# Performance work log

Hardware: AMD Instinct MI355X
Metric: run time of the kernel (lower is better)

Reference implementation:

```python
import jax, jax.numpy as jnp
import numpy as np

N_EMBD = 1024
N_HEAD = 16
HEAD_SIZE = N_EMBD // N_HEAD
EPS = 1e-5


def _layernorm(x, g, b):
    m = x.mean(-1, keepdims=True)
    v = x.var(-1, keepdims=True)
    return (x - m) / jnp.sqrt(v + EPS) * g + b


def _mha(q_in, kv_in, wq, wk, wv, pw, pb, causal):
    # q_in: [B,T,C], kv_in: [B,S,C]; per-head Linear projections fused into one matmul.
    B, T, C = q_in.shape
    S = kv_in.shape[1]
    H, hd = N_HEAD, HEAD_SIZE
    q = (q_in @ wq).reshape(B, T, H, hd)
    k = (kv_in @ wk).reshape(B, S, H, hd)
    v = (kv_in @ wv).reshape(B, S, H, hd)
    scale = 1.0 / np.sqrt(hd).astype(np.float32)
    wei = jnp.einsum('bthd,bshd->bhts', q, k) * scale  # [B,H,T,S]
    if causal:
        mask = jnp.tril(jnp.ones((T, S), dtype=bool))
        wei = jnp.where(mask, wei, -jnp.inf)
    attn = jax.nn.softmax(wei, axis=-1)
    out = jnp.einsum('bhts,bshd->bthd', attn, v).reshape(B, T, C)
    return out @ pw + pb


def setup_inputs() -> dict:
    key = jax.random.key(0)
    ks = jax.random.split(key, 20)
    C = N_EMBD
    B, T, S = 8, 1024, 1024
    s = 0.02
    inp = {
        'x': jax.random.normal(ks[0], (B, T, C), jnp.float32),
        'encoder_output': jax.random.normal(ks[1], (B, S, C), jnp.float32),
        # self-attention (per-head q/k/v Linears concatenated head-major -> [C, C])
        'sa_wq': jax.random.normal(ks[2], (C, C), jnp.float32) * s,
        'sa_wk': jax.random.normal(ks[3], (C, C), jnp.float32) * s,
        'sa_wv': jax.random.normal(ks[4], (C, C), jnp.float32) * s,
        'sa_pw': jax.random.normal(ks[5], (C, C), jnp.float32) * s,
        'sa_pb': jnp.zeros((C,), jnp.float32),
        # cross-attention
        'ca_wq': jax.random.normal(ks[6], (C, C), jnp.float32) * s,
        'ca_wk': jax.random.normal(ks[7], (C, C), jnp.float32) * s,
        'ca_wv': jax.random.normal(ks[8], (C, C), jnp.float32) * s,
        'ca_pw': jax.random.normal(ks[9], (C, C), jnp.float32) * s,
        'ca_pb': jnp.zeros((C,), jnp.float32),
        # feed-forward
        'ff_w1': jax.random.normal(ks[10], (C, 4 * C), jnp.float32) * s,
        'ff_b1': jnp.zeros((4 * C,), jnp.float32),
        'ff_w2': jax.random.normal(ks[11], (4 * C, C), jnp.float32) * s,
        'ff_b2': jnp.zeros((C,), jnp.float32),
        # layernorms
        'ln1_g': jnp.ones((C,), jnp.float32), 'ln1_b': jnp.zeros((C,), jnp.float32),
        'ln2_g': jnp.ones((C,), jnp.float32), 'ln2_b': jnp.zeros((C,), jnp.float32),
        'ln3_g': jnp.ones((C,), jnp.float32), 'ln3_b': jnp.zeros((C,), jnp.float32),
    }
    return inp


def reference(x, encoder_output, sa_wq, sa_wk, sa_wv, sa_pw, sa_pb,
              ca_wq, ca_wk, ca_wv, ca_pw, ca_pb,
              ff_w1, ff_b1, ff_w2, ff_b2,
              ln1_g, ln1_b, ln2_g, ln2_b, ln3_g, ln3_b):
    # self-attn: q from ln1(x), but k/v from raw residual x (memory=x in source)
    x = x + _mha(_layernorm(x, ln1_g, ln1_b), x, sa_wq, sa_wk, sa_wv, sa_pw, sa_pb, causal=True)
    # cross-attn: q from ln2(x), k/v from encoder_output, no mask
    x = x + _mha(_layernorm(x, ln2_g, ln2_b), encoder_output, ca_wq, ca_wk, ca_wv, ca_pw, ca_pb, causal=False)
    # feed-forward: Linear -> ReLU -> Linear
    h = _layernorm(x, ln3_g, ln3_b)
    x = x + (jax.nn.relu(h @ ff_w1 + ff_b1) @ ff_w2 + ff_b2)
    return x
```

## Files before the change

### kernel.cpp

```cpp
#include <hip/hip_runtime.h>
#include <stdint.h>
#include <stddef.h>

typedef __bf16 bf16_t;
typedef __bf16 bf16x4 __attribute__((ext_vector_type(4)));
typedef __bf16 bf16x8 __attribute__((ext_vector_type(8)));
typedef float f32x4 __attribute__((ext_vector_type(4)));

#define DEV static __device__ __forceinline__

static constexpr int kB = 8, kT = 1024, kC = 1024, kM = 8192, kH = 16, kHD = 64, kFF = 4096;

DEV f32x4 mfma16(bf16x8 a, bf16x8 b, f32x4 c) {
  return __builtin_amdgcn_mfma_f32_16x16x32_bf16(a, b, c, 0, 0, 0);
}

DEV float ex2(float x) {
  float r;
  asm("v_exp_f32 %0, %1" : "=v"(r) : "v"(x));
  return r;
}

DEV void gload_lds16(const void* g, void* l) {
  __builtin_amdgcn_global_load_lds(
      reinterpret_cast<const __attribute__((address_space(1))) void*>(
          reinterpret_cast<uintptr_t>(g)),
      reinterpret_cast<__attribute__((address_space(3))) void*>(
          static_cast<uint32_t>(reinterpret_cast<uintptr_t>(l))),
      16, 0, 0);
}

__global__ void k_cast_bf16(const float* __restrict__ in, bf16_t* __restrict__ out, int n4) {
  int i = blockIdx.x * blockDim.x + threadIdx.x;
  if (i >= n4) return;
  float4 v = reinterpret_cast<const float4*>(in)[i];
  bf16x4 o;
  o[0] = (bf16_t)v.x; o[1] = (bf16_t)v.y; o[2] = (bf16_t)v.z; o[3] = (bf16_t)v.w;
  reinterpret_cast<bf16x4*>(out)[i] = o;
}

struct Trans8Args { const float* src[8]; bf16_t* dst[8]; };
__global__ void k_transpose_cast8(Trans8Args a) {
  __shared__ float tile[32][33];
  const float* __restrict__ in = a.src[blockIdx.z];
  bf16_t* __restrict__ out = a.dst[blockIdx.z];
  int c0 = blockIdx.x * 32, r0 = blockIdx.y * 32;
  int tx = threadIdx.x, ty = threadIdx.y;
#pragma unroll
  for (int i = 0; i < 4; ++i)
    tile[ty + 8 * i][tx] = in[(size_t)(r0 + ty + 8 * i) * kC + c0 + tx];
  __syncthreads();
#pragma unroll
  for (int i = 0; i < 4; ++i)
    out[(size_t)(c0 + ty + 8 * i) * kC + r0 + tx] = (bf16_t)tile[tx][ty + 8 * i];
}

__global__ void k_transpose_cast(const float* __restrict__ in, bf16_t* __restrict__ out,
                                 int R, int C) {
  __shared__ float tile[32][33];
  int c0 = blockIdx.x * 32, r0 = blockIdx.y * 32;
  int tx = threadIdx.x, ty = threadIdx.y;
#pragma unroll
  for (int i = 0; i < 4; ++i)
    tile[ty + 8 * i][tx] = in[(size_t)(r0 + ty + 8 * i) * C + c0 + tx];
  __syncthreads();
#pragma unroll
  for (int i = 0; i < 4; ++i)
    out[(size_t)(c0 + ty + 8 * i) * R + r0 + tx] = (bf16_t)tile[tx][ty + 8 * i];
}

template <bool CASTX>
__global__ __launch_bounds__(256) void k_ln(const float* __restrict__ in,
                                            const float* __restrict__ g,
                                            const float* __restrict__ b,
                                            bf16_t* __restrict__ out,
                                            bf16_t* __restrict__ rawout) {
  int row = blockIdx.x, t = threadIdx.x;
  const float4 v = reinterpret_cast<const float4*>(in + (size_t)row * kC)[t];
  if constexpr (CASTX) {
    bf16x4 c;
    c[0] = (bf16_t)v.x; c[1] = (bf16_t)v.y; c[2] = (bf16_t)v.z; c[3] = (bf16_t)v.w;
    reinterpret_cast<bf16x4*>(rawout + (size_t)row * kC)[t] = c;
  }
  float s = v.x + v.y + v.z + v.w;
  float ss = v.x * v.x + v.y * v.y + v.z * v.z + v.w * v.w;
#pragma unroll
  for (int off = 1; off < 64; off <<= 1) {
    s += __shfl_xor(s, off, 64);
    ss += __shfl_xor(ss, off, 64);
  }
  __shared__ float rs[4], rss[4];
  int w = t >> 6;
  if ((t & 63) == 0) { rs[w] = s; rss[w] = ss; }
  __syncthreads();
  s = rs[0] + rs[1] + rs[2] + rs[3];
  ss = rss[0] + rss[1] + rss[2] + rss[3];
  float mean = s * (1.f / kC);
  float var = ss * (1.f / kC) - mean * mean;
  float rstd = rsqrtf(var + 1e-5f);
  float4 gv = reinterpret_cast<const float4*>(g)[t];
  float4 bv = reinterpret_cast<const float4*>(b)[t];
  bf16x4 o;
  o[0] = (bf16_t)((v.x - mean) * rstd * gv.x + bv.x);
  o[1] = (bf16_t)((v.y - mean) * rstd * gv.y + bv.y);
  o[2] = (bf16_t)((v.z - mean) * rstd * gv.z + bv.z);
  o[3] = (bf16_t)((v.w - mean) * rstd * gv.w + bv.w);
  reinterpret_cast<bf16x4*>(out + (size_t)row * kC)[t] = o;
}

template <int EPI, bool YFAST>
__global__ __launch_bounds__(256, 2) void k_gemm2(
    const bf16_t* __restrict__ A, const bf16_t* __restrict__ Bt,
    const float* __restrict__ bias, const float* __restrict__ res,
    float* __restrict__ outf, bf16_t* __restrict__ outb, bf16_t* __restrict__ outb2,
    int M, int N, int K) {
  extern __shared__ bf16_t smem[];
  bf16_t* As = smem;
  bf16_t* Bs = smem + 2 * 8192;
  const int t = threadIdx.x;
  const int w = t >> 6, lane = t & 63;
  const int l15 = lane & 15, l4 = lane >> 4;
  const int wr = w >> 1, wc = w & 1;

  const int gx = gridDim.x;
  const int nwg = gx * gridDim.y;
  const int lid = blockIdx.y * gx + blockIdx.x;
  const int band = lid & 7;
  const int tin = lid >> 3;
  int txi, tyi;
  if (YFAST) {
    txi = tin >> 3;
    tyi = band * 8 + (tin & 7);
  } else {
    const int tile = band * (nwg >> 3) + tin;
    txi = tile % gx;
    tyi = tile / gx;
  }
  const int bm0 = tyi * 128, bn0 = txi * 128;

  f32x4 acc[4][4] = {};

  const int srow = w * 8 + (lane >> 3);
  const int scol = ((lane & 7) ^ (lane >> 3)) * 8;
  const bf16_t* aSrc0 = A + (size_t)(bm0 + srow) * K + scol;
  const bf16_t* bSrc0 = Bt + (size_t)(bn0 + srow) * K + scol;
  const size_t r32 = (size_t)32 * K;

  const int arow = wr * 64 + l15;
  const int brow = wc * 64 + l15;
  const int cbx = (l15 & 7) * 16;
  const int cbe0 = ((l4 * 16) ^ cbx) >> 1;
  const int cbe1 = ((64 | (l4 * 16)) ^ cbx) >> 1;

  const int nkt = K >> 6;

  auto stage = [&](int tt, int bi) {
    const size_t ko = (size_t)tt * 64;
    bf16_t* da = As + bi * 8192 + w * 512;
    bf16_t* db = Bs + bi * 8192 + w * 512;
#pragma unroll
    for (int c = 0; c < 4; ++c) {
      gload_lds16(aSrc0 + ko + (size_t)c * r32, da + c * 2048);
      gload_lds16(bSrc0 + ko + (size_t)c * r32, db + c * 2048);
    }
  };

  stage(0, 0);
  asm volatile("s_waitcnt vmcnt(0)" ::: "memory");
  __builtin_amdgcn_s_barrier();

  int bi = 0;
  for (int tt = 0; tt < nkt; ++tt) {
    if (tt + 1 < nkt) stage(tt + 1, bi ^ 1);
    const bf16_t* bA = As + bi * 8192;
    const bf16_t* bB = Bs + bi * 8192;
    bf16x8 af[4], bfr[4];
#pragma unroll
    for (int m = 0; m < 4; ++m)
      af[m] = *reinterpret_cast<const bf16x8*>(&bA[(arow + m * 16) * 64 + cbe0]);
#pragma unroll
    for (int n = 0; n < 4; ++n)
      bfr[n] = *reinterpret_cast<const bf16x8*>(&bB[(brow + n * 16) * 64 + cbe0]);
    __builtin_amdgcn_s_setprio(1);
#pragma unroll
    for (int m = 0; m < 4; ++m)
#pragma unroll
      for (int n = 0; n < 4; ++n) acc[m][n] = mfma16(af[m], bfr[n], acc[m][n]);
    __builtin_amdgcn_s_setprio(0);
#pragma unroll
    for (int m = 0; m < 4; ++m)
      af[m] = *reinterpret_cast<const bf16x8*>(&bA[(arow + m * 16) * 64 + cbe1]);
#pragma unroll
    for (int n = 0; n < 4; ++n)
      bfr[n] = *reinterpret_cast<const bf16x8*>(&bB[(brow + n * 16) * 64 + cbe1]);
    __builtin_amdgcn_s_setprio(1);
#pragma unroll
    for (int m = 0; m < 4; ++m)
#pragma unroll
      for (int n = 0; n < 4; ++n) acc[m][n] = mfma16(af[m], bfr[n], acc[m][n]);
    __builtin_amdgcn_s_setprio(0);
    if (tt + 1 < nkt) {
      asm volatile("s_waitcnt vmcnt(0)" ::: "memory");
      __builtin_amdgcn_s_barrier();
    }
    bi ^= 1;
  }

  const int gm = bm0 + wr * 64 + l4 * 4;
  const int gn = bn0 + wc * 64 + l15;
  if constexpr (EPI == 0) {
#pragma unroll
    for (int m = 0; m < 4; ++m)
#pragma unroll
      for (int n = 0; n < 4; ++n)
#pragma unroll
        for (int r = 0; r < 4; ++r)
          outb[(size_t)(gm + m * 16 + r) * N + (gn + n * 16)] = (bf16_t)acc[m][n][r];
  } else if constexpr (EPI == 1) {
#pragma unroll
    for (int m = 0; m < 4; ++m)
#pragma unroll
      for (int n = 0; n < 4; ++n) {
        const int col = gn + n * 16;
        const float bv = bias[col];
#pragma unroll
        for (int r = 0; r < 4; ++r) {
          const size_t idx = (size_t)(gm + m * 16 + r) * N + col;
          outf[idx] = acc[m][n][r] + bv + res[idx];
        }
      }
  } else if constexpr (EPI == 2) {
#pragma unroll
    for (int m = 0; m < 4; ++m)
#pragma unroll
      for (int n = 0; n < 4; ++n) {
        const int col = gn + n * 16;
        const float bv = bias[col];
#pragma unroll
        for (int r = 0; r < 4; ++r) {
          float v = acc[m][n][r] + bv;
          v = fmaxf(v, 0.f);
          outb[(size_t)(gm + m * 16 + r) * N + col] = (bf16_t)v;
        }
      }
  } else if constexpr (EPI == 3) {
#pragma unroll
    for (int m = 0; m < 4; ++m)
#pragma unroll
      for (int n = 0; n < 4; ++n) {
        bf16x4 ov;
#pragma unroll
        for (int r = 0; r < 4; ++r) ov[r] = (bf16_t)acc[m][n][r];
        *reinterpret_cast<bf16x4*>(&outb[(size_t)(gn + n * 16) * M + gm + m * 16]) = ov;
      }
  } else {
    const int half = N >> 1;
    if (bn0 < half) {
#pragma unroll
      for (int m = 0; m < 4; ++m)
#pragma unroll
        for (int n = 0; n < 4; ++n)
#pragma unroll
          for (int r = 0; r < 4; ++r)
            outb[(size_t)(gm + m * 16 + r) * half + (gn + n * 16)] = (bf16_t)acc[m][n][r];
    } else {
#pragma unroll
      for (int m = 0; m < 4; ++m)
#pragma unroll
        for (int n = 0; n < 4; ++n) {
          bf16x4 ov;
#pragma unroll
          for (int r = 0; r < 4; ++r) ov[r] = (bf16_t)acc[m][n][r];
          *reinterpret_cast<bf16x4*>(
              &outb2[(size_t)(gn + n * 16 - half) * M + gm + m * 16]) = ov;
        }
    }
  }
}

template <bool CAUSAL>
__global__ __launch_bounds__(256) void k_attn(const bf16_t* __restrict__ Q,
                                              const bf16_t* __restrict__ Kb,
                                              const bf16_t* __restrict__ Vt,
                                              bf16_t* __restrict__ O) {
  __shared__ bf16_t Ks[2][4096];
  __shared__ bf16_t Vs[2][4096];
  __shared__ bf16_t P[4][32][72];
  const int b = blockIdx.x, h = blockIdx.y;
  const int w = threadIdx.x >> 6, lane = threadIdx.x & 63;
  const int l15 = lane & 15, l4 = lane >> 4;
  const int qblk = CAUSAL ? (kT / 128 - 1 - blockIdx.z) : blockIdx.z;
  const int qr0 = qblk * 128 + w * 32;

  bf16x8 qf[2][2];
#pragma unroll
  for (int a = 0; a < 2; ++a) {
    const bf16_t* qp = Q + (size_t)(b * kT + qr0 + a * 16 + l15) * kC + h * kHD + l4 * 8;
    qf[a][0] = *reinterpret_cast<const bf16x8*>(qp);
    qf[a][1] = *reinterpret_cast<const bf16x8*>(qp + 32);
#pragma unroll
    for (int j = 0; j < 8; ++j) {
      qf[a][0][j] = (bf16_t)((float)qf[a][0][j] * 0.1803368801111204f);
      qf[a][1][j] = (bf16_t)((float)qf[a][1][j] * 0.1803368801111204f);
    }
  }
  bf16x8 ones;
#pragma unroll
  for (int j = 0; j < 8; ++j) ones[j] = (bf16_t)1.0f;

  f32x4 po[2][4] = {};
  f32x4 po_s[2] = {};
  float mrun[2];
  mrun[0] = mrun[1] = -3.0e38f;

  const int nkt = CAUSAL ? 2 * qblk + 2 : (kT / 64);
  const int klim = CAUSAL ? ((qr0 + 31) >> 6) : (1 << 30);

  const int lr = lane >> 3;
  const int cswz = ((lane & 7) ^ lr) * 8;
  const bf16_t* kSrc0 = Kb + (size_t)(b * kT + 2 * w * 8 + lr) * kC + h * kHD + cswz;
  const bf16_t* kSrc1 = Kb + (size_t)(b * kT + (2 * w + 1) * 8 + lr) * kC + h * kHD + cswz;
  const bf16_t* vSrc0 = Vt + (size_t)(h * kHD + 2 * w * 8 + lr) * (kB * kT) + b * kT + cswz;
  const bf16_t* vSrc1 = Vt + (size_t)(h * kHD + (2 * w + 1) * 8 + lr) * (kB * kT) + b * kT + cswz;

  auto stage = [&](int kt, int buf) {
    const size_t kk = (size_t)kt * 64 * kC;
    const size_t vv = (size_t)kt * 64;
    gload_lds16(kSrc0 + kk, &Ks[buf][(2 * w) * 512]);
    gload_lds16(kSrc1 + kk, &Ks[buf][(2 * w + 1) * 512]);
    gload_lds16(vSrc0 + vv, &Vs[buf][(2 * w) * 512]);
    gload_lds16(vSrc1 + vv, &Vs[buf][(2 * w + 1) * 512]);
  };

  const int cbx = (l15 & 7) * 16;
  const int rb0 = ((l4 * 16) ^ cbx) >> 1;
  const int rb1 = ((64 | (l4 * 16)) ^ cbx) >> 1;

  stage(0, 0);
  asm volatile("s_waitcnt vmcnt(0)" ::: "memory");
  __builtin_amdgcn_s_barrier();

  int buf = 0;
  for (int kt = 0; kt < nkt; ++kt) {
    if (kt + 1 < nkt) stage(kt + 1, buf ^ 1);
    if (kt <= klim) {
      bf16x8 kf[4][2];
#pragma unroll
      for (int sub = 0; sub < 4; ++sub) {
        kf[sub][0] = *reinterpret_cast<const bf16x8*>(&Ks[buf][(sub * 16 + l15) * 64 + rb0]);
        kf[sub][1] = *reinterpret_cast<const bf16x8*>(&Ks[buf][(sub * 16 + l15) * 64 + rb1]);
      }
      bf16x8 vf[2][4];
#pragma unroll
      for (int n = 0; n < 4; ++n) {
        vf[0][n] = *reinterpret_cast<const bf16x8*>(&Vs[buf][(n * 16 + l15) * 64 + rb0]);
        vf[1][n] = *reinterpret_cast<const bf16x8*>(&Vs[buf][(n * 16 + l15) * 64 + rb1]);
      }

      f32x4 s[2][4] = {};
      __builtin_amdgcn_s_setprio(1);
#pragma unroll
      for (int a = 0; a < 2; ++a)
#pragma unroll
        for (int sub = 0; sub < 4; ++sub) {
          s[a][sub] = mfma16(kf[sub][0], qf[a][0], s[a][sub]);
          s[a][sub] = mfma16(kf[sub][1], qf[a][1], s[a][sub]);
        }
      __builtin_amdgcn_s_setprio(0);
      if (CAUSAL && kt == klim) {
#pragma unroll
        for (int a = 0; a < 2; ++a) {
          const int qrow = qr0 + a * 16 + l15;
#pragma unroll
          for (int sub = 0; sub < 4; ++sub)
#pragma unroll
            for (int r = 0; r < 4; ++r) {
              const int key = kt * 64 + sub * 16 + l4 * 4 + r;
              if (key > qrow) s[a][sub][r] = -3.0e38f;
            }
        }
      }
#pragma unroll
      for (int a = 0; a < 2; ++a) {
        float t0 = fmaxf(fmaxf(s[a][0][0], s[a][0][1]), fmaxf(s[a][0][2], s[a][0][3]));
        float t1 = fmaxf(fmaxf(s[a][1][0], s[a][1][1]), fmaxf(s[a][1][2], s[a][1][3]));
        float t2 = fmaxf(fmaxf(s[a][2][0], s[a][2][1]), fmaxf(s[a][2][2], s[a][2][3]));
        float t3 = fmaxf(fmaxf(s[a][3][0], s[a][3][1]), fmaxf(s[a][3][2], s[a][3][3]));
        float v = fmaxf(fmaxf(t0, t1), fmaxf(t2, t3));
        v = fmaxf(v, __shfl_xor(v, 16, 64));
        v = fmaxf(v, __shfl_xor(v, 32, 64));
        if (!__all(v <= mrun[a] + 8.f)) {
          const float mnew = fmaxf(mrun[a], v);
          const float corr = ex2(mrun[a] - mnew);
          mrun[a] = mnew;
#pragma unroll
          for (int n = 0; n < 4; ++n)
#pragma unroll
            for (int r = 0; r < 4; ++r) po[a][n][r] *= corr;
#pragma unroll
          for (int r = 0; r < 4; ++r) po_s[a][r] *= corr;
        }
#pragma unroll
        for (int sub = 0; sub < 4; ++sub) {
          bf16x4 pk;
#pragma unroll
          for (int r = 0; r < 4; ++r) pk[r] = (bf16_t)ex2(s[a][sub][r] - mrun[a]);
          *reinterpret_cast<bf16x4*>(&P[w][a * 16 + l15][sub * 16 + l4 * 4]) = pk;
        }
      }
#pragma unroll
      for (int a = 0; a < 2; ++a)
#pragma unroll
        for (int kk = 0; kk < 2; ++kk) {
          const bf16x8 pf =
              *reinterpret_cast<const bf16x8*>(&P[w][a * 16 + l15][kk * 32 + l4 * 8]);
          __builtin_amdgcn_s_setprio(1);
#pragma unroll
          for (int n = 0; n < 4; ++n) po[a][n] = mfma16(vf[kk][n], pf, po[a][n]);
          po_s[a] = mfma16(ones, pf, po_s[a]);
          __builtin_amdgcn_s_setprio(0);
        }
    }
    asm volatile("s_waitcnt vmcnt(0)" ::: "memory");
    __builtin_amdgcn_s_barrier();
    buf ^= 1;
  }

#pragma unroll
  for (int a = 0; a < 2; ++a) {
    const float inv = 1.f / po_s[a][0];
#pragma unroll
    for (int n = 0; n < 4; ++n) {
      bf16x4 ov;
#pragma unroll
      for (int r = 0; r < 4; ++r) ov[r] = (bf16_t)(po[a][n][r] * inv);
      *reinterpret_cast<bf16x4*>(
          O + (size_t)(b * kT + qr0 + a * 16 + l15) * kC + h * kHD + n * 16 + l4 * 4) = ov;
    }
  }
}

extern "C" void kernel_launch(void* const* d_in, const int* in_sizes, int n_in,
                              void* d_out, int out_size, void* d_ws, size_t ws_size,
                              hipStream_t stream) {
  const float* x      = (const float*)d_in[0];
  const float* enc    = (const float*)d_in[1];
  const float* sa_wq  = (const float*)d_in[2];
  const float* sa_wk  = (const float*)d_in[3];
  const float* sa_wv  = (const float*)d_in[4];
  const float* sa_pw  = (const float*)d_in[5];
  const float* sa_pb  = (const float*)d_in[6];
  const float* ca_wq  = (const float*)d_in[7];
  const float* ca_wk  = (const float*)d_in[8];
  const float* ca_wv  = (const float*)d_in[9];
  const float* ca_pw  = (const float*)d_in[10];
  const float* ca_pb  = (const float*)d_in[11];
  const float* ff_w1  = (const float*)d_in[12];
  const float* ff_b1  = (const float*)d_in[13];
  const float* ff_w2  = (const float*)d_in[14];
  const float* ff_b2  = (const float*)d_in[15];
  const float* ln1_g  = (const float*)d_in[16];
  const float* ln1_b  = (const float*)d_in[17];
  const float* ln2_g  = (const float*)d_in[18];
  const float* ln2_b  = (const float*)d_in[19];
  const float* ln3_g  = (const float*)d_in[20];
  const float* ln3_b  = (const float*)d_in[21];

  const size_t ACT_BF = (size_t)kM * kC * 2;
  const size_t ACT_F  = (size_t)kM * kC * 4;
  const size_t W_BF   = (size_t)kC * kC * 2;
  const size_t FF_BF  = (size_t)kC * kFF * 2;
  const size_t H_BF   = (size_t)kM * kFF * 2;

  char* ws = (char*)d_ws;
  size_t off = 0;
  auto alloc = [&](size_t bytes) {
    char* p = ws + off;
    off += (bytes + 255) & ~(size_t)255;
    return p;
  };
  bf16_t* xbf   = (bf16_t*)alloc(ACT_BF);
  bf16_t* encbf = (bf16_t*)alloc(ACT_BF);
  bf16_t* lnbuf = (bf16_t*)alloc(ACT_BF);
  bf16_t* wsaq  = (bf16_t*)alloc(W_BF);
  bf16_t* wkvsa = (bf16_t*)alloc(2 * W_BF);
  bf16_t* wsap  = (bf16_t*)alloc(W_BF);
  bf16_t* wcaq  = (bf16_t*)alloc(W_BF);
  bf16_t* wkvca = (bf16_t*)alloc(2 * W_BF);
  bf16_t* wcap  = (bf16_t*)alloc(W_BF);
  bf16_t* wff1t = (bf16_t*)alloc(FF_BF);
  bf16_t* wff2t = (bf16_t*)alloc(FF_BF);
  float*  rbuf  = (float*)alloc(ACT_F);
  char*   scr   = alloc(5 * ACT_BF > H_BF ? 5 * ACT_BF : H_BF);
  bf16_t* qbf   = (bf16_t*)scr;
  bf16_t* kbf   = (bf16_t*)(scr + ACT_BF);
  bf16_t* vtbf  = (bf16_t*)(scr + 3 * ACT_BF);
  bf16_t* aobf  = (bf16_t*)(scr + 4 * ACT_BF);
  bf16_t* hbf   = (bf16_t*)scr;

  const dim3 blk256(256), blkT(32, 8);
  const int n4 = kM * kC / 4;
  const dim3 gGemmC(kC / 128, kM / 128);
  const dim3 gGemmKV(2 * kC / 128, kM / 128);
  const dim3 gGemmF(kFF / 128, kM / 128);
  const dim3 gAttn(kB, kH, kT / 128);
  const uint32_t LDSB = 65536;

  hipFuncSetAttribute((const void*)k_gemm2<0, true>,  hipFuncAttributeMaxDynamicSharedMemorySize, LDSB);
  hipFuncSetAttribute((const void*)k_gemm2<1, true>,  hipFuncAttributeMaxDynamicSharedMemorySize, LDSB);
  hipFuncSetAttribute((const void*)k_gemm2<1, false>, hipFuncAttributeMaxDynamicSharedMemorySize, LDSB);
  hipFuncSetAttribute((const void*)k_gemm2<2, true>,  hipFuncAttributeMaxDynamicSharedMemorySize, LDSB);
  hipFuncSetAttribute((const void*)k_gemm2<4, true>,  hipFuncAttributeMaxDynamicSharedMemorySize, LDSB);

  k_cast_bf16<<<n4 / 256, blk256, 0, stream>>>(enc, encbf, n4);
  Trans8Args ta;
  ta.src[0] = sa_wq; ta.dst[0] = wsaq;
  ta.src[1] = sa_wk; ta.dst[1] = wkvsa;
  ta.src[2] = sa_wv; ta.dst[2] = wkvsa + (size_t)kC * kC;
  ta.src[3] = sa_pw; ta.dst[3] = wsap;
  ta.src[4] = ca_wq; ta.dst[4] = wcaq;
  ta.src[5] = ca_wk; ta.dst[5] = wkvca;
  ta.src[6] = ca_wv; ta.dst[6] = wkvca + (size_t)kC * kC;
  ta.src[7] = ca_pw; ta.dst[7] = wcap;
  k_transpose_cast8<<<dim3(kC / 32, kC / 32, 8), blkT, 0, stream>>>(ta);
  k_transpose_cast<<<dim3(kFF / 32, kC / 32), blkT, 0, stream>>>(ff_w1, wff1t, kC, kFF);
  k_transpose_cast<<<dim3(kC / 32, kFF / 32), blkT, 0, stream>>>(ff_w2, wff2t, kFF, kC);

  k_ln<true><<<kM, blk256, 0, stream>>>(x, ln1_g, ln1_b, lnbuf, xbf);
  k_gemm2<0, true><<<gGemmC, blk256, LDSB, stream>>>(lnbuf, wsaq, nullptr, nullptr, nullptr, qbf, nullptr, kM, kC, kC);
  k_gemm2<4, true><<<gGemmKV, blk256, LDSB, stream>>>(xbf, wkvsa, nullptr, nullptr, nullptr, kbf, vtbf, kM, 2 * kC, kC);
  k_attn<true><<<gAttn, blk256, 0, stream>>>(qbf, kbf, vtbf, aobf);
  k_gemm2<1, true><<<gGemmC, blk256, LDSB, stream>>>(aobf, wsap, sa_pb, x, rbuf, nullptr, nullptr, kM, kC, kC);

  k_ln<false><<<kM, blk256, 0, stream>>>(rbuf, ln2_g, ln2_b, lnbuf, nullptr);
  k_gemm2<0, true><<<gGemmC, blk256, LDSB, stream>>>(lnbuf, wcaq, nullptr, nullptr, nullptr, qbf, nullptr, kM, kC, kC);
  k_gemm2<4, true><<<gGemmKV, blk256, LDSB, stream>>>(encbf, wkvca, nullptr, nullptr, nullptr, kbf, vtbf, kM, 2 * kC, kC);
  k_attn<false><<<gAttn, blk256, 0, stream>>>(qbf, kbf, vtbf, aobf);
  k_gemm2<1, true><<<gGemmC, blk256, LDSB, stream>>>(aobf, wcap, ca_pb, rbuf, rbuf, nullptr, nullptr, kM, kC, kC);

  k_ln<false><<<kM, blk256, 0, stream>>>(rbuf, ln3_g, ln3_b, lnbuf, nullptr);
  k_gemm2<2, true><<<gGemmF, blk256, LDSB, stream>>>(lnbuf, wff1t, ff_b1, nullptr, nullptr, hbf, nullptr, kM, kFF, kC);
  k_gemm2<1, false><<<gGemmC, blk256, LDSB, stream>>>(hbf, wff2t, ff_b2, rbuf, (float*)d_out, nullptr, nullptr, kM, kC, kFF);

  (void)in_sizes; (void)n_in; (void)out_size; (void)ws_size;
}
```

Before: 484.8 us.

## Enlarge attention blocks to 512 threads and use nontemporal epilogue stores

Attention blocks now cover 256 query rows with eight waves, so each K/V tile staged into LDS is shared by twice as many query rows. Each wave loads one K and one V chunk per tile instead of two. GEMM and attention output stores are switched to nontemporal stores to reduce cache pollution. The risks are coarser grid granularity, causal load imbalance, and losing cache hits for outputs that the next kernel reads immediately.

```diff
diff --git a/kernel.cpp b/kernel.cpp
--- a/kernel.cpp
+++ b/kernel.cpp
@@ -215,7 +215,8 @@
       for (int n = 0; n < 4; ++n)
 #pragma unroll
         for (int r = 0; r < 4; ++r)
-          outb[(size_t)(gm + m * 16 + r) * N + (gn + n * 16)] = (bf16_t)acc[m][n][r];
+          __builtin_nontemporal_store(
+              (bf16_t)acc[m][n][r], &outb[(size_t)(gm + m * 16 + r) * N + (gn + n * 16)]);
   } else if constexpr (EPI == 1) {
 #pragma unroll
     for (int m = 0; m < 4; ++m)
@@ -226,7 +227,7 @@
 #pragma unroll
         for (int r = 0; r < 4; ++r) {
           const size_t idx = (size_t)(gm + m * 16 + r) * N + col;
-          outf[idx] = acc[m][n][r] + bv + res[idx];
+          __builtin_nontemporal_store(acc[m][n][r] + bv + res[idx], &outf[idx]);
         }
       }
   } else if constexpr (EPI == 2) {
@@ -240,7 +241,8 @@
         for (int r = 0; r < 4; ++r) {
           float v = acc[m][n][r] + bv;
           v = fmaxf(v, 0.f);
-          outb[(size_t)(gm + m * 16 + r) * N + col] = (bf16_t)v;
+          __builtin_nontemporal_store((bf16_t)v,
+                                      &outb[(size_t)(gm + m * 16 + r) * N + col]);
         }
       }
   } else if constexpr (EPI == 3) {
@@ -251,7 +253,8 @@
         bf16x4 ov;
 #pragma unroll
         for (int r = 0; r < 4; ++r) ov[r] = (bf16_t)acc[m][n][r];
-        *reinterpret_cast<bf16x4*>(&outb[(size_t)(gn + n * 16) * M + gm + m * 16]) = ov;
+        __builtin_nontemporal_store(
+            ov, reinterpret_cast<bf16x4*>(&outb[(size_t)(gn + n * 16) * M + gm + m * 16]));
       }
   } else {
     const int half = N >> 1;
@@ -262,7 +265,9 @@
         for (int n = 0; n < 4; ++n)
 #pragma unroll
           for (int r = 0; r < 4; ++r)
-            outb[(size_t)(gm + m * 16 + r) * half + (gn + n * 16)] = (bf16_t)acc[m][n][r];
+            __builtin_nontemporal_store(
+                (bf16_t)acc[m][n][r],
+                &outb[(size_t)(gm + m * 16 + r) * half + (gn + n * 16)]);
     } else {
 #pragma unroll
       for (int m = 0; m < 4; ++m)
@@ -271,26 +276,27 @@
           bf16x4 ov;
 #pragma unroll
           for (int r = 0; r < 4; ++r) ov[r] = (bf16_t)acc[m][n][r];
-          *reinterpret_cast<bf16x4*>(
-              &outb2[(size_t)(gn + n * 16 - half) * M + gm + m * 16]) = ov;
+          __builtin_nontemporal_store(
+              ov, reinterpret_cast<bf16x4*>(
+                      &outb2[(size_t)(gn + n * 16 - half) * M + gm + m * 16]));
         }
     }
   }
 }
 
 template <bool CAUSAL>
-__global__ __launch_bounds__(256) void k_attn(const bf16_t* __restrict__ Q,
+__global__ __launch_bounds__(512) void k_attn(const bf16_t* __restrict__ Q,
                                               const bf16_t* __restrict__ Kb,
                                               const bf16_t* __restrict__ Vt,
                                               bf16_t* __restrict__ O) {
   __shared__ bf16_t Ks[2][4096];
   __shared__ bf16_t Vs[2][4096];
-  __shared__ bf16_t P[4][32][72];
+  __shared__ bf16_t P[8][32][72];
   const int b = blockIdx.x, h = blockIdx.y;
   const int w = threadIdx.x >> 6, lane = threadIdx.x & 63;
   const int l15 = lane & 15, l4 = lane >> 4;
-  const int qblk = CAUSAL ? (kT / 128 - 1 - blockIdx.z) : blockIdx.z;
-  const int qr0 = qblk * 128 + w * 32;
+  const int qseg = CAUSAL ? (kT / 256 - 1 - blockIdx.z) : blockIdx.z;
+  const int qr0 = qseg * 256 + w * 32;
 
   bf16x8 qf[2][2];
 #pragma unroll
@@ -313,23 +319,17 @@
   float mrun[2];
   mrun[0] = mrun[1] = -3.0e38f;
 
-  const int nkt = CAUSAL ? 2 * qblk + 2 : (kT / 64);
+  const int nkt = CAUSAL ? 4 * qseg + 4 : (kT / 64);
   const int klim = CAUSAL ? ((qr0 + 31) >> 6) : (1 << 30);
 
   const int lr = lane >> 3;
   const int cswz = ((lane & 7) ^ lr) * 8;
-  const bf16_t* kSrc0 = Kb + (size_t)(b * kT + 2 * w * 8 + lr) * kC + h * kHD + cswz;
-  const bf16_t* kSrc1 = Kb + (size_t)(b * kT + (2 * w + 1) * 8 + lr) * kC + h * kHD + cswz;
-  const bf16_t* vSrc0 = Vt + (size_t)(h * kHD + 2 * w * 8 + lr) * (kB * kT) + b * kT + cswz;
-  const bf16_t* vSrc1 = Vt + (size_t)(h * kHD + (2 * w + 1) * 8 + lr) * (kB * kT) + b * kT + cswz;
+  const bf16_t* kSrc = Kb + (size_t)(b * kT + w * 8 + lr) * kC + h * kHD + cswz;
+  const bf16_t* vSrc = Vt + (size_t)(h * kHD + w * 8 + lr) * (kB * kT) + b * kT + cswz;
 
   auto stage = [&](int kt, int buf) {
-    const size_t kk = (size_t)kt * 64 * kC;
-    const size_t vv = (size_t)kt * 64;
-    gload_lds16(kSrc0 + kk, &Ks[buf][(2 * w) * 512]);
-    gload_lds16(kSrc1 + kk, &Ks[buf][(2 * w + 1) * 512]);
-    gload_lds16(vSrc0 + vv, &Vs[buf][(2 * w) * 512]);
-    gload_lds16(vSrc1 + vv, &Vs[buf][(2 * w + 1) * 512]);
+    gload_lds16(kSrc + (size_t)kt * 64 * kC, &Ks[buf][w * 512]);
+    gload_lds16(vSrc + (size_t)kt * 64,      &Vs[buf][w * 512]);
   };
 
   const int cbx = (l15 & 7) * 16;
@@ -434,8 +434,9 @@
       bf16x4 ov;
 #pragma unroll
       for (int r = 0; r < 4; ++r) ov[r] = (bf16_t)(po[a][n][r] * inv);
-      *reinterpret_cast<bf16x4*>(
-          O + (size_t)(b * kT + qr0 + a * 16 + l15) * kC + h * kHD + n * 16 + l4 * 4) = ov;
+      __builtin_nontemporal_store(
+          ov, reinterpret_cast<bf16x4*>(
+                  O + (size_t)(b * kT + qr0 + a * 16 + l15) * kC + h * kHD + n * 16 + l4 * 4));
     }
   }
 }
@@ -498,12 +499,12 @@
   bf16_t* aobf  = (bf16_t*)(scr + 4 * ACT_BF);
   bf16_t* hbf   = (bf16_t*)scr;
 
-  const dim3 blk256(256), blkT(32, 8);
+  const dim3 blk512(512), blk256(256), blkT(32, 8);
   const int n4 = kM * kC / 4;
   const dim3 gGemmC(kC / 128, kM / 128);
   const dim3 gGemmKV(2 * kC / 128, kM / 128);
   const dim3 gGemmF(kFF / 128, kM / 128);
-  const dim3 gAttn(kB, kH, kT / 128);
+  const dim3 gAttn(kB, kH, kT / 256);
   const uint32_t LDSB = 65536;
 
   hipFuncSetAttribute((const void*)k_gemm2<0, true>,  hipFuncAttributeMaxDynamicSharedMemorySize, LDSB);
@@ -529,13 +530,13 @@
   k_ln<true><<<kM, blk256, 0, stream>>>(x, ln1_g, ln1_b, lnbuf, xbf);
   k_gemm2<0, true><<<gGemmC, blk256, LDSB, stream>>>(lnbuf, wsaq, nullptr, nullptr, nullptr, qbf, nullptr, kM, kC, kC);
   k_gemm2<4, true><<<gGemmKV, blk256, LDSB, stream>>>(xbf, wkvsa, nullptr, nullptr, nullptr, kbf, vtbf, kM, 2 * kC, kC);
-  k_attn<true><<<gAttn, blk256, 0, stream>>>(qbf, kbf, vtbf, aobf);
+  k_attn<true><<<gAttn, blk512, 0, stream>>>(qbf, kbf, vtbf, aobf);
   k_gemm2<1, true><<<gGemmC, blk256, LDSB, stream>>>(aobf, wsap, sa_pb, x, rbuf, nullptr, nullptr, kM, kC, kC);
 
   k_ln<false><<<kM, blk256, 0, stream>>>(rbuf, ln2_g, ln2_b, lnbuf, nullptr);
   k_gemm2<0, true><<<gGemmC, blk256, LDSB, stream>>>(lnbuf, wcaq, nullptr, nullptr, nullptr, qbf, nullptr, kM, kC, kC);
   k_gemm2<4, true><<<gGemmKV, blk256, LDSB, stream>>>(encbf, wkvca, nullptr, nullptr, nullptr, kbf, vtbf, kM, 2 * kC, kC);
-  k_attn<false><<<gAttn, blk256, 0, stream>>>(qbf, kbf, vtbf, aobf);
+  k_attn<false><<<gAttn, blk512, 0, stream>>>(qbf, kbf, vtbf, aobf);
   k_gemm2<1, true><<<gGemmC, blk256, LDSB, stream>>>(aobf, wcap, ca_pb, rbuf, rbuf, nullptr, nullptr, kM, kC, kC);
 
   k_ln<false><<<kM, blk256, 0, stream>>>(rbuf, ln3_g, ln3_b, lnbuf, nullptr);
```

New measurement: 516.6 us. +6.6%, slower.
